# Performance work log

Measured on AMD Instinct MI355X. Metric: run time of the kernel, lower is better.

The kernel has to match this reference:

```python
import jax, jax.numpy as jnp
import numpy as np

IMG = 224; P = 16; C = 3
G = IMG // P; N = G * G            # 14, 196 patches
DIM = 768; DEPTH = 6; HEADS = 12; DH = 64; MLP = 3072
INNER = HEADS * DH                  # 768
PD = C * P * P                      # 768 patch_dim
B = 32


def _coords():
    m, n = np.meshgrid(np.arange(G), np.arange(G))
    return jnp.asarray(np.stack((m, n), axis=-1).reshape(-1, 2), jnp.float32)  # (N,2)


def _ln(x, g, b, eps=1e-5):
    mu = jnp.mean(x, -1, keepdims=True)
    var = jnp.mean((x - mu) ** 2, -1, keepdims=True)
    return (x - mu) * jax.lax.rsqrt(var + eps) * g + b


def setup_inputs() -> dict:
    key = jax.random.key(0)
    ks = jax.random.split(key, 16)
    s = 0.02
    inp = {
        "img": jax.random.normal(ks[0], (B, C, IMG, IMG), jnp.float32),
        "noise_token": jnp.zeros((1,), jnp.float32),
        "A_noise": jax.random.normal(ks[1], (B, 2, 2), jnp.float32),
        "b_noise": jax.random.normal(ks[2], (B, 2), jnp.float32),
        "A_mean": jnp.eye(2, dtype=jnp.float32),
        "b_mean": jnp.zeros((2,), jnp.float32),
        "A_std": jnp.zeros((2, 2), jnp.float32),   # variance_init=0.0
        "b_std": jnp.zeros((2,), jnp.float32),
        "band_width": jnp.asarray(1.0, jnp.float32),
        "Wp": jax.random.normal(ks[3], (PD, DIM), jnp.float32) * s,
        "bp": jnp.zeros((DIM,), jnp.float32),
        "ln1_g": jnp.ones((DEPTH, DIM), jnp.float32),
        "ln1_b": jnp.zeros((DEPTH, DIM), jnp.float32),
        "Wqkv": jax.random.normal(ks[4], (DEPTH, DIM, 3 * INNER), jnp.float32) * s,
        "Wout": jax.random.normal(ks[5], (DEPTH, INNER, DIM), jnp.float32) * s,
        "bout": jnp.zeros((DEPTH, DIM), jnp.float32),
        "ln2_g": jnp.ones((DEPTH, DIM), jnp.float32),
        "ln2_b": jnp.zeros((DEPTH, DIM), jnp.float32),
        "Wff1": jax.random.normal(ks[6], (DEPTH, DIM, MLP), jnp.float32) * s,
        "bff1": jnp.zeros((DEPTH, MLP), jnp.float32),
        "Wff2": jax.random.normal(ks[7], (DEPTH, MLP, DIM), jnp.float32) * s,
        "bff2": jnp.zeros((DEPTH, DIM), jnp.float32),
        "Wep": jax.random.normal(ks[8], (DIM, PD), jnp.float32) * s,
        "bep": jnp.zeros((PD,), jnp.float32),
    }
    return inp


def reference(img, noise_token, A_noise, b_noise, A_mean, b_mean, A_std, b_std,
              band_width, Wp, bp, ln1_g, ln1_b, Wqkv, Wout, bout,
              ln2_g, ln2_b, Wff1, bff1, Wff2, bff2, Wep, bep):
    del noise_token  # deleted in the original forward
    b = img.shape[0]
    X = _coords()  # (N,2) base patch grid coords, non-trainable buffer
    # patchify: b c (h p1) (w p2) -> b (h w) (p1 p2 c)
    x = img.reshape(b, C, G, P, G, P).transpose(0, 2, 4, 3, 5, 1).reshape(b, N, PD)
    x = x @ Wp + bp
    # stochastic affine transform of coordinates
    A = A_mean + jax.nn.softplus(A_std) * A_noise          # (b,2,2)
    bt = b_mean + jax.nn.softplus(b_std) * b_noise         # (b,2)
    Xt = jnp.einsum('pd,bdo->bpo', X, A) + bt[:, None, :]  # (b,N,2)
    # RBF attention scores: dots[b,i,j] = -||Xt[b,j] - X[i]||^2 / band_width
    diff = Xt[:, None, :, :] - X[None, :, None, :]         # (b,N,N,2)
    dots = -jnp.sum(diff ** 2, axis=-1) / band_width       # (b,N,N)
    attn = jax.nn.softmax(dots, axis=-1)                   # same for all heads/layers
    for l in range(DEPTH):
        y = _ln(x, ln1_g[l], ln1_b[l])
        qkv = y @ Wqkv[l]                                  # q,k unused (pos_only=True)
        v = qkv[..., 2 * INNER:].reshape(b, N, HEADS, DH).transpose(0, 2, 1, 3)
        o = jnp.einsum('bij,bhjd->bhid', attn, v)
        o = o.transpose(0, 2, 1, 3).reshape(b, N, INNER)
        x = o @ Wout[l] + bout[l]                          # NOTE: no residual on attention (matches source)
        h = _ln(x, ln2_g[l], ln2_b[l])
        h = jax.nn.gelu(h @ Wff1[l] + bff1[l], approximate=False) @ Wff2[l] + bff2[l]
        x = x + h
    x = x @ Wep + bep
    # un-patchify: b (h w) (p1 p2 c) -> b c (h p1) (w p2)
    out = x.reshape(b, G, G, P, P, C).transpose(0, 5, 1, 3, 2, 4).reshape(b, C, IMG, IMG)
    return out
```

## Files before the change

kernel.cpp:

```cpp
#include <hip/hip_runtime.h>
#include <hip/hip_bf16.h>
#include <math.h>

#define NTOK 196
#define KPAD 224
#define BATCH 32
#define ROWS (BATCH * NTOK)
#define DIMC 768
#define MLPD 3072

typedef __hip_bfloat16 bf16;
typedef short bf16x8 __attribute__((ext_vector_type(8)));
typedef float f32x4 __attribute__((ext_vector_type(4)));

__device__ __forceinline__ void gload16(const void* g, void* l) {
    __builtin_amdgcn_global_load_lds(
        (__attribute__((address_space(1))) void*)const_cast<void*>(g),
        (__attribute__((address_space(3))) void*)l, 16, 0, 0);
}

__device__ __forceinline__ float softplus_f(float x) {
    return fmaxf(x, 0.f) + log1pf(expf(-fabsf(x)));
}
__device__ __forceinline__ float gelu_f(float x) {
    return 0.5f * x * (1.f + erff(x * 0.70710678118654752f));
}
__device__ __forceinline__ float to_f(float x) { return x; }
__device__ __forceinline__ float to_f(bf16 x) { return __bfloat162float(x); }

__global__ __launch_bounds__(64) void attn_kernel(
    const float* __restrict__ A_noise, const float* __restrict__ b_noise,
    const float* __restrict__ A_mean,  const float* __restrict__ b_mean,
    const float* __restrict__ A_std,   const float* __restrict__ b_std,
    const float* __restrict__ bwp, bf16* __restrict__ attn)
{
    int bi = blockIdx.x;
    int b = bi / NTOK, i = bi % NTOK;
    int lane = threadIdx.x;
    float A00 = A_mean[0] + softplus_f(A_std[0]) * A_noise[b * 4 + 0];
    float A01 = A_mean[1] + softplus_f(A_std[1]) * A_noise[b * 4 + 1];
    float A10 = A_mean[2] + softplus_f(A_std[2]) * A_noise[b * 4 + 2];
    float A11 = A_mean[3] + softplus_f(A_std[3]) * A_noise[b * 4 + 3];
    float bt0 = b_mean[0] + softplus_f(b_std[0]) * b_noise[b * 2 + 0];
    float bt1 = b_mean[1] + softplus_f(b_std[1]) * b_noise[b * 2 + 1];
    float inv_bw = 1.f / bwp[0];
    float Xi0 = (float)(i % 14), Xi1 = (float)(i / 14);
    float d[4];
    float mx = -1e30f;
    #pragma unroll
    for (int r = 0; r < 4; ++r) {
        int j = lane + r * 64;
        if (j < NTOK) {
            float Xj0 = (float)(j % 14), Xj1 = (float)(j / 14);
            float t0 = Xj0 * A00 + Xj1 * A10 + bt0 - Xi0;
            float t1 = Xj0 * A01 + Xj1 * A11 + bt1 - Xi1;
            d[r] = -(t0 * t0 + t1 * t1) * inv_bw;
            mx = fmaxf(mx, d[r]);
        } else d[r] = -1e30f;
    }
    for (int off = 1; off < 64; off <<= 1) mx = fmaxf(mx, __shfl_xor(mx, off));
    float e[4]; float s = 0.f;
    #pragma unroll
    for (int r = 0; r < 4; ++r) {
        int j = lane + r * 64;
        e[r] = (j < NTOK) ? expf(d[r] - mx) : 0.f;
        s += e[r];
    }
    for (int off = 1; off < 64; off <<= 1) s += __shfl_xor(s, off);
    float inv = 1.f / s;
    bf16* row = attn + (long)bi * KPAD;
    #pragma unroll
    for (int r = 0; r < 4; ++r) {
        int j = lane + r * 64;
        if (j < KPAD) row[j] = __float2bfloat16(j < NTOK ? e[r] * inv : 0.f);
    }
}

__global__ __launch_bounds__(256) void patchify_kernel(
    const float* __restrict__ img, bf16* __restrict__ Xp)
{
    long idx = (long)blockIdx.x * 256 + threadIdx.x;
    if (idx >= (long)ROWS * DIMC) return;
    int pd = (int)(idx % DIMC); long r = idx / DIMC;
    int n = (int)(r % NTOK); int b = (int)(r / NTOK);
    int c = pd % 3; int pp = pd / 3; int p2 = pp % 16; int p1 = pp / 16;
    int gw = n % 14, gh = n / 14;
    int h = gh * 16 + p1, w = gw * 16 + p2;
    Xp[idx] = __float2bfloat16(img[(((long)b * 3 + c) * 224 + h) * 224 + w]);
}

__global__ __launch_bounds__(256) void unpatchify_kernel(
    const float* __restrict__ xe, float* __restrict__ out)
{
    long idx = (long)blockIdx.x * 256 + threadIdx.x;
    if (idx >= (long)BATCH * 3 * 224 * 224) return;
    int w = (int)(idx % 224); long r = idx / 224;
    int h = (int)(r % 224); r /= 224;
    int c = (int)(r % 3); int b = (int)(r / 3);
    int gh = h / 16, p1 = h % 16, gw = w / 16, p2 = w % 16;
    int n = gh * 14 + gw;
    int pd = (p1 * 16 + p2) * 3 + c;
    out[idx] = xe[((long)b * NTOK + n) * DIMC + pd];
}

__global__ __launch_bounds__(256) void ln_kernel(
    const float* __restrict__ x, const float* __restrict__ g,
    const float* __restrict__ bb, bf16* __restrict__ y)
{
    int row = blockIdx.x;
    const float* xr = x + (long)row * DIMC;
    bf16* yr = y + (long)row * DIMC;
    int t = threadIdx.x;
    float v0 = xr[t], v1 = xr[t + 256], v2 = xr[t + 512];
    float s = v0 + v1 + v2;
    float s2 = v0 * v0 + v1 * v1 + v2 * v2;
    for (int off = 32; off; off >>= 1) { s += __shfl_down(s, off); s2 += __shfl_down(s2, off); }
    __shared__ float ps[4], ps2[4];
    if ((t & 63) == 0) { ps[t >> 6] = s; ps2[t >> 6] = s2; }
    __syncthreads();
    float S = ps[0] + ps[1] + ps[2] + ps[3];
    float S2 = ps2[0] + ps2[1] + ps2[2] + ps2[3];
    float mean = S * (1.f / DIMC);
    float var = S2 * (1.f / DIMC) - mean * mean;
    float rs = rsqrtf(var + 1e-5f);
    yr[t]       = __float2bfloat16((v0 - mean) * rs * g[t]       + bb[t]);
    yr[t + 256] = __float2bfloat16((v1 - mean) * rs * g[t + 256] + bb[t + 256]);
    yr[t + 512] = __float2bfloat16((v2 - mean) * rs * g[t + 512] + bb[t + 512]);
}

template<typename TIN>
__global__ __launch_bounds__(256) void transpose_cvt(
    const TIN* __restrict__ in, bf16* __restrict__ out,
    int R, int C, int ldin, int ldout, int Rpad, long sIn, long sOut)
{
    __shared__ float tile[32][33];
    in  += (long)blockIdx.z * sIn;
    out += (long)blockIdx.z * sOut;
    int c0 = blockIdx.x * 32, r0 = blockIdx.y * 32;
    int tx = threadIdx.x & 31, ty = threadIdx.x >> 5;
    #pragma unroll
    for (int i = 0; i < 32; i += 8) {
        int r = r0 + ty + i, c = c0 + tx;
        float v = 0.f;
        if (r < R && c < C) v = to_f(in[(long)r * ldin + c]);
        tile[ty + i][tx] = v;
    }
    __syncthreads();
    #pragma unroll
    for (int i = 0; i < 32; i += 8) {
        int c = c0 + ty + i, r = r0 + tx;
        if (c < C && r < Rpad) out[(long)c * ldout + r] = __float2bfloat16(tile[tx][ty + i]);
    }
}

__global__ __launch_bounds__(256) void cvt_kernel(const float* __restrict__ in,
                                                  bf16* __restrict__ out, int n)
{
    int i = blockIdx.x * 256 + threadIdx.x;
    if (i < n) out[i] = __float2bfloat16(in[i]);
}

__global__ __launch_bounds__(256) void cvt_wv_kernel(const float* __restrict__ Wqkv,
                                                     bf16* __restrict__ out)
{
    long i = (long)blockIdx.x * 256 + threadIdx.x;
    if (i >= 6L * 768 * 768) return;
    int c = (int)(i % 768); long rl = i / 768;
    int r = (int)(rl % 768); int l = (int)(rl / 768);
    out[i] = __float2bfloat16(Wqkv[((long)l * 768 + r) * 2304 + 1536 + c]);
}

template<int BN, int ACT, int ACCUM, int OUTF32, int GUARDM>
__global__ __launch_bounds__(256) void gemm_bf16(
    const bf16* __restrict__ A, const bf16* __restrict__ Bt,
    const float* __restrict__ bias, void* __restrict__ Cv,
    int M, int K, int lda, int ldb, int ldc,
    long sA, long sB, long sC)
{
    constexpr int FN = BN / 32;
    __shared__ __align__(16) char smem[32768];
    bf16* As = (bf16*)smem;
    bf16* Bs = (bf16*)(smem + 16384);
    A  += (long)blockIdx.z * sA;
    Bt += (long)blockIdx.z * sB;
    const int m0 = blockIdx.y * 128, n0 = blockIdx.x * BN;
    const int t = threadIdx.x, wave = t >> 6, lane = t & 63;
    const int lrow = t >> 2, lcol = (t & 3) * 8;
    const bf16* ag = A  + (long)(m0 + lrow) * lda + lcol;
    const bf16* bg = Bt + (long)(n0 + lrow) * ldb + lcol;
    bf16* asw = As + wave * 512;
    bf16* bsw = Bs + wave * 512;
    const int fr = lane & 15, kq = lane >> 4;
    const int wr = wave >> 1, wc = wave & 1;
    f32x4 acc[4][FN];
    #pragma unroll
    for (int m = 0; m < 4; ++m)
        #pragma unroll
        for (int n = 0; n < FN; ++n) acc[m][n] = (f32x4){0.f, 0.f, 0.f, 0.f};

    const int nt = K >> 5;
    gload16(ag, asw);
    gload16(ag + 64 * (long)lda, asw + 2048);
    gload16(bg, bsw);
    if (BN == 128) gload16(bg + 64 * (long)ldb, bsw + 2048);
    __syncthreads();
    for (int it = 0; it < nt; ++it) {
        const int cur = it & 1;
        if (it + 1 < nt) {
            const int k0 = (it + 1) << 5;
            const int nb = cur ^ 1;
            gload16(ag + k0, asw + nb * 4096);
            gload16(ag + 64 * (long)lda + k0, asw + nb * 4096 + 2048);
            gload16(bg + k0, bsw + nb * (BN * 32));
            if (BN == 128) gload16(bg + 64 * (long)ldb + k0, bsw + nb * (BN * 32) + 2048);
        }
        const bf16* as = As + cur * 4096;
        const bf16* bs = Bs + cur * (BN * 32);
        bf16x8 af[4], bfv[FN];
        #pragma unroll
        for (int m = 0; m < 4; ++m)
            af[m] = *(const bf16x8*)&as[(wr * 64 + m * 16 + fr) * 32 + kq * 8];
        #pragma unroll
        for (int n = 0; n < FN; ++n)
            bfv[n] = *(const bf16x8*)&bs[(wc * (BN / 2) + n * 16 + fr) * 32 + kq * 8];
        #pragma unroll
        for (int m = 0; m < 4; ++m)
            #pragma unroll
            for (int n = 0; n < FN; ++n)
                acc[m][n] = __builtin_amdgcn_mfma_f32_16x16x32_bf16(af[m], bfv[n], acc[m][n], 0, 0, 0);
        __syncthreads();
    }

    const int rbase = kq * 4;
    if constexpr (OUTF32) {
        static_assert(BN == 64, "f32 epilogue assumes BN=64 (32KB LDS)");
        float* Cs = (float*)smem;
        #pragma unroll
        for (int n = 0; n < FN; ++n) {
            int lc = wc * (BN / 2) + n * 16 + fr;
            float bi = bias ? bias[n0 + lc] : 0.f;
            #pragma unroll
            for (int m = 0; m < 4; ++m)
                #pragma unroll
                for (int r = 0; r < 4; ++r) {
                    int lr = wr * 64 + m * 16 + rbase + r;
                    float vv = acc[m][n][r] + bi;
                    if (ACT) vv = gelu_f(vv);
                    Cs[lr * BN + lc] = vv;
                }
        }
        __syncthreads();
        float* Cp = (float*)Cv + (long)blockIdx.z * sC;
        #pragma unroll
        for (int i = 0; i < (128 * BN) / (256 * 4); ++i) {
            int chunk = i * 256 + t;
            int row = chunk / (BN / 4), c4 = (chunk % (BN / 4)) * 4;
            int gm = m0 + row;
            if (GUARDM && gm >= M) continue;
            float4 v4 = *(const float4*)&Cs[row * BN + c4];
            float* p = Cp + (long)gm * ldc + n0 + c4;
            if (ACCUM) {
                float4 o4 = *(const float4*)p;
                v4.x += o4.x; v4.y += o4.y; v4.z += o4.z; v4.w += o4.w;
            }
            *(float4*)p = v4;
        }
    } else {
        bf16* Cs = (bf16*)smem;
        #pragma unroll
        for (int n = 0; n < FN; ++n) {
            int lc = wc * (BN / 2) + n * 16 + fr;
            float bi = bias ? bias[n0 + lc] : 0.f;
            #pragma unroll
            for (int m = 0; m < 4; ++m)
                #pragma unroll
                for (int r = 0; r < 4; ++r) {
                    int lr = wr * 64 + m * 16 + rbase + r;
                    float vv = acc[m][n][r] + bi;
                    if (ACT) vv = gelu_f(vv);
                    Cs[lr * BN + lc] = __float2bfloat16(vv);
                }
        }
        __syncthreads();
        bf16* Cp = (bf16*)Cv + (long)blockIdx.z * sC;
        #pragma unroll
        for (int i = 0; i < (128 * BN) / (256 * 8); ++i) {
            int chunk = i * 256 + t;
            int row = chunk / (BN / 8), c8 = (chunk % (BN / 8)) * 8;
            int gm = m0 + row;
            if (GUARDM && gm >= M) continue;
            *(bf16x8*)(Cp + (long)gm * ldc + n0 + c8) = *(const bf16x8*)&Cs[row * BN + c8];
        }
    }
}

extern "C" void kernel_launch(void* const* d_in, const int* in_sizes, int n_in,
                              void* d_out, int out_size, void* d_ws, size_t ws_size,
                              hipStream_t stream) {
    const float* img     = (const float*)d_in[0];
    const float* A_noise = (const float*)d_in[2];
    const float* b_noise = (const float*)d_in[3];
    const float* A_mean  = (const float*)d_in[4];
    const float* b_mean  = (const float*)d_in[5];
    const float* A_std   = (const float*)d_in[6];
    const float* b_std   = (const float*)d_in[7];
    const float* band_w  = (const float*)d_in[8];
    const float* Wp      = (const float*)d_in[9];
    const float* bp      = (const float*)d_in[10];
    const float* ln1_g   = (const float*)d_in[11];
    const float* ln1_b   = (const float*)d_in[12];
    const float* Wqkv    = (const float*)d_in[13];
    const float* Wout    = (const float*)d_in[14];
    const float* bout    = (const float*)d_in[15];
    const float* ln2_g   = (const float*)d_in[16];
    const float* ln2_b   = (const float*)d_in[17];
    const float* Wff1    = (const float*)d_in[18];
    const float* bff1    = (const float*)d_in[19];
    const float* Wff2    = (const float*)d_in[20];
    const float* bff2    = (const float*)d_in[21];
    const float* Wep     = (const float*)d_in[22];
    const float* bep     = (const float*)d_in[23];
    float* out = (float*)d_out;

    char* w = (char*)d_ws;
    bf16* WpT  = (bf16*)w; w += 768L * 768 * 2;
    bf16* WepT = (bf16*)w; w += 768L * 768 * 2;
    bf16* WvoT = (bf16*)w; w += 6L * 768 * 768 * 2;
    bf16* Wf1T = (bf16*)w; w += 6L * 3072 * 768 * 2;
    bf16* Wf2T = (bf16*)w; w += 6L * 768 * 3072 * 2;
    bf16* attnb = (bf16*)w; w += (long)(ROWS + 64) * KPAD * 2;
    bf16* Xpb  = (bf16*)w; w += (long)ROWS * DIMC * 2;
    bf16* yb   = (bf16*)w; w += (long)ROWS * DIMC * 2;
    bf16* yTb  = (bf16*)w; w += (long)BATCH * DIMC * KPAD * 2;
    bf16* ya   = (bf16*)w; w += (long)ROWS * DIMC * 2;
    bf16* h1b  = (bf16*)w; w += (long)ROWS * MLPD * 2;
    float* x   = (float*)w; w += (long)ROWS * DIMC * 4;
    bf16* WoT  = h1b;
    bf16* Wvb  = h1b + 6L * 768 * 768;

    transpose_cvt<float><<<dim3(24, 24, 1), 256, 0, stream>>>(Wp,  WpT,  768, 768, 768, 768, 768, 0, 0);
    transpose_cvt<float><<<dim3(24, 24, 1), 256, 0, stream>>>(Wep, WepT, 768, 768, 768, 768, 768, 0, 0);
    transpose_cvt<float><<<dim3(24, 24, 6), 256, 0, stream>>>(Wout, WoT, 768, 768, 768, 768, 768,
                                                              768L * 768, 768L * 768);
    cvt_wv_kernel<<<(int)((6L * 768 * 768 + 255) / 256), 256, 0, stream>>>(Wqkv, Wvb);
    transpose_cvt<float><<<dim3(96, 24, 6), 256, 0, stream>>>(Wff1, Wf1T, 768, 3072, 3072, 768, 768,
                                                              768L * 3072, 3072L * 768);
    transpose_cvt<float><<<dim3(24, 96, 6), 256, 0, stream>>>(Wff2, Wf2T, 3072, 768, 768, 3072, 3072,
                                                              3072L * 768, 768L * 3072);
    gemm_bf16<64, 0, 0, 0, 0><<<dim3(12, 6, 6), 256, 0, stream>>>(
        WoT, Wvb, nullptr, WvoT, 768, 768, 768, 768, 768,
        768L * 768, 768L * 768, 768L * 768);

    attn_kernel<<<ROWS, 64, 0, stream>>>(A_noise, b_noise, A_mean, b_mean, A_std, b_std, band_w, attnb);

    patchify_kernel<<<(ROWS * DIMC + 255) / 256, 256, 0, stream>>>(img, Xpb);
    gemm_bf16<64, 0, 0, 1, 0><<<dim3(12, 49, 1), 256, 0, stream>>>(
        Xpb, WpT, bp, x, ROWS, 768, 768, 768, 768, 0, 0, 0);

    for (int l = 0; l < 6; ++l) {
        ln_kernel<<<ROWS, 256, 0, stream>>>(x, ln1_g + l * 768, ln1_b + l * 768, yb);
        transpose_cvt<bf16><<<dim3(24, 7, 32), 256, 0, stream>>>(
            yb, yTb, NTOK, 768, 768, KPAD, KPAD, (long)NTOK * 768, (long)768 * KPAD);
        gemm_bf16<64, 0, 0, 0, 1><<<dim3(12, 2, BATCH), 256, 0, stream>>>(
            attnb, yTb, nullptr, ya, NTOK, KPAD, KPAD, KPAD, 768,
            (long)NTOK * KPAD, (long)768 * KPAD, (long)NTOK * 768);
        gemm_bf16<64, 0, 0, 1, 0><<<dim3(12, 49, 1), 256, 0, stream>>>(
            ya, WvoT + (long)l * 768 * 768, bout + l * 768, x, ROWS, 768, 768, 768, 768, 0, 0, 0);
        ln_kernel<<<ROWS, 256, 0, stream>>>(x, ln2_g + l * 768, ln2_b + l * 768, yb);
        gemm_bf16<128, 1, 0, 0, 0><<<dim3(24, 49, 1), 256, 0, stream>>>(
            yb, Wf1T + (long)l * 3072 * 768, bff1 + l * 3072, h1b, ROWS, 768, 768, 768, 3072, 0, 0, 0);
        gemm_bf16<64, 0, 1, 1, 0><<<dim3(12, 49, 1), 256, 0, stream>>>(
            h1b, Wf2T + (long)l * 768 * 3072, bff2 + l * 768, x, ROWS, 3072, 3072, 3072, 768, 0, 0, 0);
    }

    bf16* xb = Xpb;
    float* xe = (float*)h1b;
    cvt_kernel<<<(ROWS * DIMC + 255) / 256, 256, 0, stream>>>(x, xb, ROWS * DIMC);
    gemm_bf16<64, 0, 0, 1, 0><<<dim3(12, 49, 1), 256, 0, stream>>>(
        xb, WepT, bep, xe, ROWS, 768, 768, 768, 768, 0, 0, 0);
    unpatchify_kernel<<<(BATCH * 3 * 224 * 224 + 255) / 256, 256, 0, stream>>>(xe, out);
}
```

Before: 1.251 ms.

## Triple-buffer GEMM LDS tiles with vmcnt-based waits and MFMA priority

The bf16 GEMM moves from a double-buffered loop with a full __syncthreads per k-step to a three-stage LDS ring. Loads are issued two tiles ahead, and the loop waits only on the older loads via s_waitcnt vmcnt plus a raw s_barrier. It also raises wave priority around the MFMA block. The goal is to hide global-to-LDS latency behind compute, at the cost of more LDS per block (36–48 KB), which may lower occupancy.

```diff
diff --git a/kernel.cpp b/kernel.cpp
--- a/kernel.cpp
+++ b/kernel.cpp
@@ -178,9 +178,12 @@
     long sA, long sB, long sC)
 {
     constexpr int FN = BN / 32;
-    __shared__ __align__(16) char smem[32768];
+    constexpr int LPT = 2 + BN / 64;
+    constexpr int BSTRIDE = BN * 32;
+    constexpr int SMEM = (BN == 128) ? 49152 : 36864;
+    __shared__ __align__(16) char smem[SMEM];
     bf16* As = (bf16*)smem;
-    bf16* Bs = (bf16*)(smem + 16384);
+    bf16* Bs = (bf16*)(smem + 3 * 8192);
     A  += (long)blockIdx.z * sA;
     Bt += (long)blockIdx.z * sB;
     const int m0 = blockIdx.y * 128, n0 = blockIdx.x * BN;
@@ -188,8 +191,6 @@
     const int lrow = t >> 2, lcol = (t & 3) * 8;
     const bf16* ag = A  + (long)(m0 + lrow) * lda + lcol;
     const bf16* bg = Bt + (long)(n0 + lrow) * ldb + lcol;
-    bf16* asw = As + wave * 512;
-    bf16* bsw = Bs + wave * 512;
     const int fr = lane & 15, kq = lane >> 4;
     const int wr = wave >> 1, wc = wave & 1;
     f32x4 acc[4][FN];
@@ -198,24 +199,18 @@
         #pragma unroll
         for (int n = 0; n < FN; ++n) acc[m][n] = (f32x4){0.f, 0.f, 0.f, 0.f};
 
-    const int nt = K >> 5;
-    gload16(ag, asw);
-    gload16(ag + 64 * (long)lda, asw + 2048);
-    gload16(bg, bsw);
-    if (BN == 128) gload16(bg + 64 * (long)ldb, bsw + 2048);
-    __syncthreads();
-    for (int it = 0; it < nt; ++it) {
-        const int cur = it & 1;
-        if (it + 1 < nt) {
-            const int k0 = (it + 1) << 5;
-            const int nb = cur ^ 1;
-            gload16(ag + k0, asw + nb * 4096);
-            gload16(ag + 64 * (long)lda + k0, asw + nb * 4096 + 2048);
-            gload16(bg + k0, bsw + nb * (BN * 32));
-            if (BN == 128) gload16(bg + 64 * (long)ldb + k0, bsw + nb * (BN * 32) + 2048);
-        }
-        const bf16* as = As + cur * 4096;
-        const bf16* bs = Bs + cur * (BN * 32);
+    auto stage = [&](int kt, int bufi) {
+        const int k0 = kt << 5;
+        bf16* ab = As + bufi * 4096 + wave * 512;
+        bf16* bb = Bs + bufi * BSTRIDE + wave * 512;
+        gload16(ag + k0, ab);
+        gload16(ag + 64 * (long)lda + k0, ab + 2048);
+        gload16(bg + k0, bb);
+        if constexpr (BN == 128) gload16(bg + 64 * (long)ldb + k0, bb + 2048);
+    };
+    auto compute = [&](int bufi) {
+        const bf16* as = As + bufi * 4096;
+        const bf16* bs = Bs + bufi * BSTRIDE;
         bf16x8 af[4], bfv[FN];
         #pragma unroll
         for (int m = 0; m < 4; ++m)
@@ -223,17 +218,37 @@
         #pragma unroll
         for (int n = 0; n < FN; ++n)
             bfv[n] = *(const bf16x8*)&bs[(wc * (BN / 2) + n * 16 + fr) * 32 + kq * 8];
+        __builtin_amdgcn_s_setprio(1);
         #pragma unroll
         for (int m = 0; m < 4; ++m)
             #pragma unroll
             for (int n = 0; n < FN; ++n)
                 acc[m][n] = __builtin_amdgcn_mfma_f32_16x16x32_bf16(af[m], bfv[n], acc[m][n], 0, 0, 0);
-        __syncthreads();
-    }
+        __builtin_amdgcn_s_setprio(0);
+    };
+
+    const int nt = K >> 5;
+    stage(0, 0);
+    stage(1, 1);
+    int cur = 0, pf = 2;
+    for (int it = 0; it < nt - 1; ++it) {
+        asm volatile("s_waitcnt vmcnt(%0)" :: "n"(LPT) : "memory");
+        __builtin_amdgcn_s_barrier();
+        __builtin_amdgcn_sched_barrier(0);
+        if (it + 2 < nt) stage(it + 2, pf);
+        compute(cur);
+        cur = (cur == 2) ? 0 : cur + 1;
+        pf  = (pf  == 2) ? 0 : pf + 1;
+    }
+    asm volatile("s_waitcnt vmcnt(0)" ::: "memory");
+    __builtin_amdgcn_s_barrier();
+    __builtin_amdgcn_sched_barrier(0);
+    compute(cur);
+    __syncthreads();
 
     const int rbase = kq * 4;
     if constexpr (OUTF32) {
-        static_assert(BN == 64, "f32 epilogue assumes BN=64 (32KB LDS)");
+        static_assert(BN == 64, "f32 epilogue assumes BN=64");
         float* Cs = (float*)smem;
         #pragma unroll
         for (int n = 0; n < FN; ++n) {
```

Result: no change. 1.239 ms (-0.9%).
